# Kernel tuning notes

Hardware: AMD Instinct MI355X
Metric: run time of the kernel (lower is better)

The kernel has to match this reference:

```python
import jax, jax.numpy as jnp
import numpy as np

B, T, C = 2, 2048, 1024
H = 16
DH = C // H  # 64
DFF = 4 * C  # 4096
EPS = 1e-5


def layernorm(x, gamma, beta):
    # torch.var defaults to unbiased (ddof=1) -- replicate exactly
    m = jnp.mean(x, axis=-1, keepdims=True)
    v = jnp.var(x, axis=-1, ddof=1, keepdims=True)
    return (x - m) / jnp.sqrt(v + EPS) * gamma + beta


def setup_inputs() -> dict:
    key = jax.random.key(0)
    ks = jax.random.split(key, 12)
    s = 0.02
    return {
        "x": jax.random.normal(ks[0], (B, T, C), jnp.float32),
        "Wq": jax.random.normal(ks[1], (H, C, DH), jnp.float32) * s,
        "bq": jnp.zeros((H, DH), jnp.float32),
        "Wk": jax.random.normal(ks[2], (H, C, DH), jnp.float32) * s,
        "bk": jnp.zeros((H, DH), jnp.float32),
        "Wv": jax.random.normal(ks[3], (H, C, DH), jnp.float32) * s,
        "bv": jnp.zeros((H, DH), jnp.float32),
        "Wo": jax.random.normal(ks[4], (C, C), jnp.float32) * s,
        "bo": jnp.zeros((C,), jnp.float32),
        "gamma1": jnp.ones((C,), jnp.float32),
        "beta1": jnp.zeros((C,), jnp.float32),
        "gamma2": jnp.ones((C,), jnp.float32),
        "beta2": jnp.zeros((C,), jnp.float32),
        "W1": jax.random.normal(ks[5], (C, DFF), jnp.float32) * s,
        "b1": jnp.zeros((DFF,), jnp.float32),
        "W2": jax.random.normal(ks[6], (DFF, C), jnp.float32) * s,
        "b2": jnp.zeros((C,), jnp.float32),
    }


def reference(x, Wq, bq, Wk, bk, Wv, bv, Wo, bo,
              gamma1, beta1, gamma2, beta2, W1, b1, W2, b2):
    Tn = x.shape[1]
    # Block: x = ln1(x); x = x + attn(x); x = ln2(x); out = x + ffw(x)
    x = layernorm(x, gamma1, beta1)

    # per-head Q/K/V linears, stacked over heads: [B,T,C] x [H,C,Dh] -> [B,H,T,Dh]
    q = jnp.einsum('btc,hcd->bhtd', x, Wq) + bq[None, :, None, :]
    k = jnp.einsum('btc,hcd->bhtd', x, Wk) + bk[None, :, None, :]
    v = jnp.einsum('btc,hcd->bhtd', x, Wv) + bv[None, :, None, :]

    scale = DH ** -0.5
    scores = jnp.einsum('bhtd,bhsd->bhts', q, k) * scale  # [B,H,T,T]
    causal = jnp.tril(jnp.ones((Tn, Tn), dtype=bool))
    scores = jnp.where(causal, scores, -jnp.inf)
    alpha = jax.nn.softmax(scores, axis=-1)
    h = jnp.einsum('bhts,bhsd->bhtd', alpha, v)  # [B,H,T,Dh]
    h = jnp.transpose(h, (0, 2, 1, 3)).reshape(x.shape)  # concat heads -> [B,T,C]
    attn_out = h @ Wo + bo

    x = x + attn_out
    x = layernorm(x, gamma2, beta2)
    ffw = jax.nn.gelu(x @ W1 + b1, approximate=False) @ W2 + b2
    return x + ffw
```

## Files before the change

### kernel.cpp

```cpp
#include <hip/hip_runtime.h>

typedef unsigned short u16;
typedef unsigned int u32;
typedef __attribute__((ext_vector_type(8))) short bf16x8;
typedef __attribute__((ext_vector_type(4))) float f32x4;

#define AS1 __attribute__((address_space(1)))
#define AS3 __attribute__((address_space(3)))

__device__ __forceinline__ u16 f2bf(float f) {
  u32 u = __float_as_uint(f);
  u = (u + 0x7fffu + ((u >> 16) & 1u)) >> 16;
  return (u16)u;
}
__device__ __forceinline__ float bf2f(u16 v) { return __uint_as_float((u32)v << 16); }

__device__ __forceinline__ void gl16(const void* g, void* l) {
  __builtin_amdgcn_global_load_lds((AS1 void*)g, (AS3 void*)l, 16, 0, 0);
}

__device__ __forceinline__ float exp2a(float x) {
  float r;
  asm("v_exp_f32 %0, %1" : "=v"(r) : "v"(x));
  return r;
}
__device__ __forceinline__ u32 pk2(float lo, float hi) {
  u32 r;
  asm("v_cvt_pk_bf16_f32 %0, %1, %2" : "=v"(r) : "v"(lo), "v"(hi));
  return r;
}

#define BAR() __builtin_amdgcn_s_barrier()
#define LGKM0()                                         \
  do {                                                  \
    asm volatile("s_waitcnt lgkmcnt(0)" ::: "memory");  \
    __builtin_amdgcn_sched_barrier(0);                  \
  } while (0)
#define VMC4()                                          \
  do {                                                  \
    asm volatile("s_waitcnt vmcnt(4)" ::: "memory");    \
    __builtin_amdgcn_sched_barrier(0);                  \
  } while (0)
#define VMC0()                                          \
  do {                                                  \
    asm volatile("s_waitcnt vmcnt(0)" ::: "memory");    \
    __builtin_amdgcn_sched_barrier(0);                  \
  } while (0)

__global__ __launch_bounds__(256) void ln_kernel(const float* __restrict__ in,
                                                 const float* __restrict__ gamma,
                                                 const float* __restrict__ beta,
                                                 u16* __restrict__ obf,
                                                 float* __restrict__ of32) {
  const int row = blockIdx.x;
  const int tid = threadIdx.x;
  const float* xr = in + (long)row * 1024;
  float4 v = *(const float4*)(xr + tid * 4);
  float s = v.x + v.y + v.z + v.w;
  float sq = v.x * v.x + v.y * v.y + v.z * v.z + v.w * v.w;
#pragma unroll
  for (int off = 1; off < 64; off <<= 1) {
    s += __shfl_xor(s, off);
    sq += __shfl_xor(sq, off);
  }
  __shared__ float rs[4], rq[4];
  const int w = tid >> 6, lane = tid & 63;
  if (lane == 0) { rs[w] = s; rq[w] = sq; }
  __syncthreads();
  s = rs[0] + rs[1] + rs[2] + rs[3];
  sq = rq[0] + rq[1] + rq[2] + rq[3];
  const float mean = s * (1.0f / 1024.0f);
  const float var = (sq - 1024.0f * mean * mean) * (1.0f / 1023.0f);
  const float rstd = rsqrtf(var + 1e-5f);
  float4 g4 = *(const float4*)(gamma + tid * 4);
  float4 b4 = *(const float4*)(beta + tid * 4);
  float o0 = (v.x - mean) * rstd * g4.x + b4.x;
  float o1 = (v.y - mean) * rstd * g4.y + b4.y;
  float o2 = (v.z - mean) * rstd * g4.z + b4.z;
  float o3 = (v.w - mean) * rstd * g4.w + b4.w;
  *(float4*)(of32 + (long)row * 1024 + tid * 4) = make_float4(o0, o1, o2, o3);
  ushort4 ub;
  ub.x = f2bf(o0); ub.y = f2bf(o1); ub.z = f2bf(o2); ub.w = f2bf(o3);
  *(ushort4*)(obf + (long)row * 1024 + tid * 4) = ub;
}

__global__ __launch_bounds__(256) void ln2_fused_kernel(
    const u16* __restrict__ p0, const u16* __restrict__ p1,
    const float* __restrict__ bo, const float* __restrict__ xn,
    const float* __restrict__ gamma, const float* __restrict__ beta,
    u16* __restrict__ obf, float* __restrict__ of32) {
  const int row = blockIdx.x;
  const int tid = threadIdx.x;
  const long i4 = (long)row * 1024 + tid * 4;
  ushort4 a0 = *(const ushort4*)(p0 + i4);
  ushort4 a1 = *(const ushort4*)(p1 + i4);
  float4 xv = *(const float4*)(xn + i4);
  float4 bv = *(const float4*)(bo + tid * 4);
  float y0 = bf2f(a0.x) + bf2f(a1.x) + bv.x + xv.x;
  float y1 = bf2f(a0.y) + bf2f(a1.y) + bv.y + xv.y;
  float y2 = bf2f(a0.z) + bf2f(a1.z) + bv.z + xv.z;
  float y3 = bf2f(a0.w) + bf2f(a1.w) + bv.w + xv.w;
  float s = y0 + y1 + y2 + y3;
  float sq = y0 * y0 + y1 * y1 + y2 * y2 + y3 * y3;
#pragma unroll
  for (int off = 1; off < 64; off <<= 1) {
    s += __shfl_xor(s, off);
    sq += __shfl_xor(sq, off);
  }
  __shared__ float rs[4], rq[4];
  const int w = tid >> 6, lane = tid & 63;
  if (lane == 0) { rs[w] = s; rq[w] = sq; }
  __syncthreads();
  s = rs[0] + rs[1] + rs[2] + rs[3];
  sq = rq[0] + rq[1] + rq[2] + rq[3];
  const float mean = s * (1.0f / 1024.0f);
  const float var = (sq - 1024.0f * mean * mean) * (1.0f / 1023.0f);
  const float rstd = rsqrtf(var + 1e-5f);
  float4 g4 = *(const float4*)(gamma + tid * 4);
  float4 b4 = *(const float4*)(beta + tid * 4);
  float o0 = (y0 - mean) * rstd * g4.x + b4.x;
  float o1 = (y1 - mean) * rstd * g4.y + b4.y;
  float o2 = (y2 - mean) * rstd * g4.z + b4.z;
  float o3 = (y3 - mean) * rstd * g4.w + b4.w;
  *(float4*)(of32 + i4) = make_float4(o0, o1, o2, o3);
  ushort4 ub;
  ub.x = f2bf(o0); ub.y = f2bf(o1); ub.z = f2bf(o2); ub.w = f2bf(o3);
  *(ushort4*)(obf + i4) = ub;
}

__global__ __launch_bounds__(256) void wtrans_kernel(const float* __restrict__ in,
                                                     u16* __restrict__ out,
                                                     int R, int C, int in_rs,
                                                     long in_batch, long out_batch) {
  __shared__ float tile[32][33];
  const float* ip = in + (long)blockIdx.z * in_batch;
  u16* op = out + (long)blockIdx.z * out_batch;
  const int c0 = blockIdx.x * 32, r0 = blockIdx.y * 32;
  const int tx = threadIdx.x, ty = threadIdx.y;
#pragma unroll
  for (int i = 0; i < 4; ++i)
    tile[ty + i * 8][tx] = ip[(long)(r0 + ty + i * 8) * in_rs + c0 + tx];
  __syncthreads();
#pragma unroll
  for (int i = 0; i < 4; ++i)
    op[(long)(c0 + ty + i * 8) * R + r0 + tx] = f2bf(tile[tx][ty + i * 8]);
}

__device__ __forceinline__ void mfma_phase(f32x4 acc[8][4], const bf16x8 af[4][2],
                                           const bf16x8 bf[2][2], int mq, int nq) {
#pragma unroll
  for (int mf = 0; mf < 4; ++mf)
#pragma unroll
    for (int nf = 0; nf < 2; ++nf)
#pragma unroll
      for (int kh = 0; kh < 2; ++kh)
        acc[mq * 4 + mf][nq * 2 + nf] = __builtin_amdgcn_mfma_f32_16x16x32_bf16(
            af[mf][kh], bf[nf][kh], acc[mq * 4 + mf][nq * 2 + nf], 0, 0, 0);
}

#define STGA(BUFX)                                          \
  do {                                                      \
    gl16(pA0, Asm + (BUFX) * 16384 + tid * 8);              \
    gl16(pA1, Asm + (BUFX) * 16384 + 4096 + tid * 8);       \
    gl16(pA2, Asm + (BUFX) * 16384 + 8192 + tid * 8);       \
    gl16(pA3, Asm + (BUFX) * 16384 + 12288 + tid * 8);      \
  } while (0)
#define STGB(BUFX)                                          \
  do {                                                      \
    gl16(pB0, Bsm + (BUFX) * 16384 + tid * 8);              \
    gl16(pB1, Bsm + (BUFX) * 16384 + 4096 + tid * 8);       \
    gl16(pB2, Bsm + (BUFX) * 16384 + 8192 + tid * 8);       \
    gl16(pB3, Bsm + (BUFX) * 16384 + 12288 + tid * 8);      \
  } while (0)
#define ADVA() do { pA0 += 64; pA1 += 64; pA2 += 64; pA3 += 64; } while (0)
#define ADVB() do { pB0 += 64; pB1 += 64; pB2 += 64; pB3 += 64; } while (0)

#define RD(arr, off) (*(const bf16x8*)((arr) + (off)))

#define KTILE(BUF, T)                                                        \
  do {                                                                       \
    bf16x8 af[4][2], b0[2][2], b1[2][2];                                     \
    _Pragma("unroll") for (int mf = 0; mf < 4; ++mf)                         \
        _Pragma("unroll") for (int kh = 0; kh < 2; ++kh)                     \
            af[mf][kh] = RD(Asm, aO[mf][kh] + (BUF) * 16384);                \
    _Pragma("unroll") for (int nf = 0; nf < 2; ++nf)                         \
        _Pragma("unroll") for (int kh = 0; kh < 2; ++kh)                     \
            b0[nf][kh] = RD(Bsm, bO[nf][kh] + (BUF) * 16384);                \
    if ((T) + 1 < nk) STGA((BUF) ^ 1);                                       \
    BAR(); LGKM0();                                                          \
    __builtin_amdgcn_s_setprio(1);                                           \
    mfma_phase(acc, af, b0, 0, 0);                                           \
    __builtin_amdgcn_s_setprio(0);                                           \
    BAR();                                                                   \
    _Pragma("unroll") for (int nf = 0; nf < 2; ++nf)                         \
        _Pragma("unroll") for (int kh = 0; kh < 2; ++kh)                     \
            b1[nf][kh] = RD(Bsm, bO[nf][kh] + (BUF) * 16384 + 2048);         \
    BAR(); LGKM0();                                                          \
    __builtin_amdgcn_s_setprio(1);                                           \
    mfma_phase(acc, af, b1, 0, 1);                                           \
    __builtin_amdgcn_s_setprio(0);                                           \
    BAR();                                                                   \
    _Pragma("unroll") for (int mf = 0; mf < 4; ++mf)                         \
        _Pragma("unroll") for (int kh = 0; kh < 2; ++kh)                     \
            af[mf][kh] = RD(Asm, aO[mf][kh] + (BUF) * 16384 + 4096);         \
    if ((T) + 2 < nk) STGB(BUF);                                             \
    BAR(); LGKM0();                                                          \
    __builtin_amdgcn_s_setprio(1);                                           \
    mfma_phase(acc, af, b0, 1, 0);                                           \
    __builtin_amdgcn_s_setprio(0);                                           \
    BAR();                                                                   \
    if ((T) + 2 < nk) { VMC4(); } else { VMC0(); }                           \
    BAR();                                                                   \
    __builtin_amdgcn_s_setprio(1);                                           \
    mfma_phase(acc, af, b1, 1, 1);                                           \
    __builtin_amdgcn_s_setprio(0);                                           \
    BAR();                                                                   \
  } while (0)

template <int EPI>
__global__ __launch_bounds__(512, 2) void gemm8_kernel(
    const u16* __restrict__ A, const u16* __restrict__ Bt,
    int lda, int ldb, int M, int N, int nk,
    const float* bias0, const float* bias1, const float* bias2,
    void* out0, void* out1) {
  __shared__ __align__(16) u16 Asm[4 * 8192];
  __shared__ __align__(16) u16 Bsm[4 * 8192];
  const int tid = threadIdx.x;
  const int lane = tid & 63, w = tid >> 6;
  const int wm = w >> 2, wn = w & 3;
  const int q15 = lane & 15, g = lane >> 4;

  const int nbx = gridDim.x, nby = gridDim.y;
  const int nwg = nbx * nby * gridDim.z;
  int lid = blockIdx.x + nbx * (blockIdx.y + nby * blockIdx.z);
  lid = (lid & 7) * (nwg >> 3) + (lid >> 3);
  const int bx = lid % nbx;
  const int rest = lid / nbx;
  const int by = rest % nby;
  const int bz = rest / nby;

  const long m0 = (long)bx * 256;
  const long n0 = (long)by * 256;
  const long koff = (long)bz * (long)nk * 64;
  const u16* Ab = A + m0 * lda + koff;
  const u16* Bb = Bt + n0 * ldb + koff;

  const int jr = tid >> 3;
  const int js = ((tid & 7) ^ (jr & 7)) * 8;
  const u16* pA0 = Ab + (long)jr * lda + js;
  const u16* pA1 = pA0 + (long)64 * lda;
  const u16* pA2 = pA0 + (long)128 * lda;
  const u16* pA3 = pA0 + (long)192 * lda;
  const u16* pB0 = Bb + (long)jr * ldb + js;
  const u16* pB1 = pB0 + (long)64 * ldb;
  const u16* pB2 = pB0 + (long)128 * ldb;
  const u16* pB3 = pB0 + (long)192 * ldb;

  int aO[4][2], bO[2][2];
#pragma unroll
  for (int mf = 0; mf < 4; ++mf)
#pragma unroll
    for (int kh = 0; kh < 2; ++kh) {
      const int rh = mf * 16 + q15;
      aO[mf][kh] = wm * 8192 + rh * 64 + (((kh * 4 + g) ^ (rh & 7)) * 8);
    }
  const int brow = (wn & 1) * 64;
#pragma unroll
  for (int nf = 0; nf < 2; ++nf)
#pragma unroll
    for (int kh = 0; kh < 2; ++kh) {
      const int rh = brow + nf * 16 + q15;
      bO[nf][kh] = (wn >> 1) * 8192 + rh * 64 + (((kh * 4 + g) ^ (rh & 7)) * 8);
    }

  f32x4 acc[8][4];
  f32x4 zero4 = {0.f, 0.f, 0.f, 0.f};
#pragma unroll
  for (int mi = 0; mi < 8; ++mi)
#pragma unroll
    for (int ni = 0; ni < 4; ++ni) acc[mi][ni] = zero4;

  STGA(0);
  STGB(0);
  ADVB();
  if (nk > 1) {
    STGB(1);
    VMC4();
  } else {
    VMC0();
  }
  ADVA();
  ADVB();
  BAR();

  for (int tt = 0; tt < nk; tt += 2) {
    KTILE(0, tt);
    ADVA(); ADVB();
    KTILE(1, tt + 1);
    ADVA(); ADVB();
  }

#pragma unroll
  for (int mi = 0; mi < 8; ++mi) {
#pragma unroll
    for (int ni = 0; ni < 4; ++ni) {
      const long mbase = m0 + wm * 128 + (mi >> 2) * 64 + (mi & 3) * 16 + 4 * g;
      const long n = n0 + wn * 64 + (ni >> 1) * 32 + (ni & 1) * 16 + q15;
      f32x4 a = acc[mi][ni];
      if constexpr (EPI == 0) {
        const int sel = (int)(n >> 10);
        const int nn = (int)(n & 1023);
        const float* bp = sel == 0 ? bias0 : (sel == 1 ? bias1 : bias2);
        const float bb2 = bp[nn];
        if (sel < 2) {
          const float sc = (sel == 0) ? 0.18033688011112043f : 1.0f;
          u16* qkp = (u16*)out0;
#pragma unroll
          for (int r = 0; r < 4; ++r)
            qkp[(mbase + r) * 2048 + n] = f2bf((a[r] + bb2) * sc);
        } else {
          const int bI = (int)(mbase >> 11);
          const int t = (int)(mbase & 2047);
          const int hh = nn >> 6, dh = nn & 63;
          ushort4 pk;
          pk.x = f2bf(a[0] + bb2); pk.y = f2bf(a[1] + bb2);
          pk.z = f2bf(a[2] + bb2); pk.w = f2bf(a[3] + bb2);
          *(ushort4*)((u16*)out1 + ((long)((bI * 16 + hh) * 64 + dh)) * 2048 + t) = pk;
        }
      } else if constexpr (EPI == 2) {
        u16* gp = (u16*)out0;
        const float bb2 = bias0[(int)n];
#pragma unroll
        for (int r = 0; r < 4; ++r) {
          const float xg = a[r] + bb2;
          const float ge = 0.5f * xg * (1.0f + erff(xg * 0.70710678118f));
          gp[(mbase + r) * N + n] = f2bf(ge);
        }
      } else {
        u16* pp = (u16*)out0 + (long)bz * M * N;
#pragma unroll
        for (int r = 0; r < 4; ++r) pp[(mbase + r) * N + n] = f2bf(a[r]);
      }
    }
  }
}

__global__ __launch_bounds__(256) void ffn2_reduce_kernel(const u16* __restrict__ p,
                                                          const float* __restrict__ b2,
                                                          const float* __restrict__ yn,
                                                          float* __restrict__ out) {
  const long i4 = ((long)blockIdx.x * 256 + threadIdx.x) * 4;
  ushort4 p0 = *(const ushort4*)(p + i4);
  ushort4 p1 = *(const ushort4*)(p + 4194304 + i4);
  ushort4 p2 = *(const ushort4*)(p + 8388608 + i4);
  ushort4 p3 = *(const ushort4*)(p + 12582912 + i4);
  float4 rr = *(const float4*)(yn + i4);
  const int nn = (int)(i4 & 1023);
  float4 bb = *(const float4*)(b2 + nn);
  float4 o;
  o.x = bf2f(p0.x) + bf2f(p1.x) + bf2f(p2.x) + bf2f(p3.x) + bb.x + rr.x;
  o.y = bf2f(p0.y) + bf2f(p1.y) + bf2f(p2.y) + bf2f(p3.y) + bb.y + rr.y;
  o.z = bf2f(p0.z) + bf2f(p1.z) + bf2f(p2.z) + bf2f(p3.z) + bb.z + rr.z;
  o.w = bf2f(p0.w) + bf2f(p1.w) + bf2f(p2.w) + bf2f(p3.w) + bb.w + rr.w;
  *(float4*)(out + i4) = o;
}

__global__ __launch_bounds__(256, 2) void gemm_wo_kernel(const u16* __restrict__ A,
                                                         const u16* __restrict__ Bt,
                                                         u16* __restrict__ part) {
  __shared__ __align__(16) u16 Asm[128 * 64];
  __shared__ __align__(16) u16 Bsm[128 * 64];
  const int tid = threadIdx.x;
  const int lane = tid & 63, w = tid >> 6;
  const int wm = w >> 1, wn = w & 1;
  const int q = lane & 15, g = lane >> 4;
  const long m0 = (long)blockIdx.x * 128;
  const long n0 = (long)blockIdx.y * 128;
  const int bz = blockIdx.z;
  const long koff = (long)bz * 512;

  f32x4 zero4 = {0.f, 0.f, 0.f, 0.f};
  f32x4 acc[4][4];
#pragma unroll
  for (int mi = 0; mi < 4; ++mi)
#pragma unroll
    for (int ni = 0; ni < 4; ++ni) acc[mi][ni] = zero4;

  for (int ks = 0; ks < 8; ++ks) {
    __syncthreads();
    const u16* ga = A + m0 * 1024 + koff + ks * 64;
    const u16* gb = Bt + n0 * 1024 + koff + ks * 64;
    const int base = w * 256;
#pragma unroll
    for (int i = 0; i < 4; ++i) {
      const int idx = base + i * 64 + lane;
      const int row = idx >> 3;
      const int lg = (idx & 7) ^ (row & 7);
      gl16(ga + (long)row * 1024 + lg * 8, Asm + (long)(base + i * 64) * 8);
    }
#pragma unroll
    for (int i = 0; i < 4; ++i) {
      const int idx = base + i * 64 + lane;
      const int row = idx >> 3;
      const int lg = (idx & 7) ^ (row & 7);
      gl16(gb + (long)row * 1024 + lg * 8, Bsm + (long)(base + i * 64) * 8);
    }
    __syncthreads();
#pragma unroll
    for (int half = 0; half < 2; ++half) {
      bf16x8 af[4], bfv[4];
#pragma unroll
      for (int mi = 0; mi < 4; ++mi) {
        const int row = wm * 64 + mi * 16 + q;
        const int ph = (half * 4 + g) ^ (row & 7);
        af[mi] = *(const bf16x8*)(Asm + row * 64 + ph * 8);
      }
#pragma unroll
      for (int ni = 0; ni < 4; ++ni) {
        const int row = wn * 64 + ni * 16 + q;
        const int ph = (half * 4 + g) ^ (row & 7);
        bfv[ni] = *(const bf16x8*)(Bsm + row * 64 + ph * 8);
      }
#pragma unroll
      for (int mi = 0; mi < 4; ++mi)
#pragma unroll
        for (int ni = 0; ni < 4; ++ni)
          acc[mi][ni] = __builtin_amdgcn_mfma_f32_16x16x32_bf16(af[mi], bfv[ni],
                                                                acc[mi][ni], 0, 0, 0);
    }
  }
  u16* pp = part + (long)bz * 4096 * 1024;
#pragma unroll
  for (int mi = 0; mi < 4; ++mi) {
#pragma unroll
    for (int ni = 0; ni < 4; ++ni) {
      const long mbase = m0 + wm * 64 + mi * 16 + 4 * g;
      const long n = n0 + wn * 64 + ni * 16 + q;
      f32x4 a = acc[mi][ni];
#pragma unroll
      for (int r = 0; r < 4; ++r) pp[(mbase + r) * 1024 + n] = f2bf(a[r]);
    }
  }
}

__device__ __forceinline__ void attn_stage(const u16* kbase, const u16* vtb, int kb,
                                           u16* Kd, u16* Vd, int tid) {
#pragma unroll
  for (int it = 0; it < 2; ++it) {
    const int j = it * 256 + tid;
    const int row = j >> 3;
    const int lg = (j & 7) ^ (row & 7);
    gl16(kbase + (long)(kb * 64 + row) * 2048 + lg * 8, Kd + j * 8);
    gl16(vtb + (long)row * 2048 + kb * 64 + lg * 8, Vd + j * 8);
  }
}

__device__ __forceinline__ void softmax_slab(const f32x4 st[4], bool diag, int qrow,
                                             int kb, int g, int q15,
                                             float& m2, float& l, u16* prow,
                                             float al[4]) {
  float sv[4][4];
  float rmax = -1e30f;
#pragma unroll
  for (int sub = 0; sub < 4; ++sub)
#pragma unroll
    for (int r = 0; r < 4; ++r) {
      float s_ = st[sub][r];
      if (diag) {
        const int key = kb * 64 + sub * 16 + 4 * g + r;
        s_ = (key > qrow) ? -1e30f : s_;
      }
      sv[sub][r] = s_;
      rmax = fmaxf(rmax, s_);
    }
  rmax = fmaxf(rmax, __shfl_xor(rmax, 16));
  rmax = fmaxf(rmax, __shfl_xor(rmax, 32));
  const float mnew = fmaxf(m2, rmax);
  const float alpha = exp2a(m2 - mnew);
  float psum = 0.f;
#pragma unroll
  for (int sub = 0; sub < 4; ++sub) {
    const float p0 = exp2a(sv[sub][0] - mnew);
    const float p1 = exp2a(sv[sub][1] - mnew);
    const float p2 = exp2a(sv[sub][2] - mnew);
    const float p3 = exp2a(sv[sub][3] - mnew);
    uint2 u;
    u.x = pk2(p0, p1);
    u.y = pk2(p2, p3);
    *(uint2*)(prow + sub * 16 + 4 * g) = u;
    psum += (p0 + p1) + (p2 + p3);
  }
  psum += __shfl_xor(psum, 16);
  psum += __shfl_xor(psum, 32);
  l = l * alpha + psum;
  m2 = mnew;
#pragma unroll
  for (int r = 0; r < 4; ++r) al[r] = __shfl(alpha, 4 * g + r);
}

__global__ __launch_bounds__(256, 2) void attn_kernel(const u16* __restrict__ qk,
                                                      const u16* __restrict__ vT,
                                                      u16* __restrict__ o) {
  __shared__ __align__(16) u16 Ksm[2][64 * 64];
  __shared__ __align__(16) u16 Vsm[2][64 * 64];
  __shared__ __align__(16) u16 Psm[8][16][72];
  const int lid = blockIdx.x;
  const int xcd = lid & 7, s6 = lid >> 3;
  const int b2 = (s6 >> 4) & 3, xr = s6 & 15;
  const int qs = (b2 & 2) ? (15 - xr) : xr;
  const int bh = xcd + 8 * b2;
  const int b = bh >> 4, h = bh & 15;
  const int tid = threadIdx.x, lane = tid & 63, w = tid >> 6;
  const int q15 = lane & 15, g = lane >> 4;
  const u16* qbase = qk + (long)b * 2048 * 2048 + h * 64;
  const u16* kbase = qbase + 1024;
  const u16* vtb = vT + (long)bh * 64 * 2048;
  f32x4 zero4 = {0.f, 0.f, 0.f, 0.f};

  const int r0 = qs * 128 + w * 16 + q15;
  bf16x8 qa[2][2];
  qa[0][0] = *(const bf16x8*)(qbase + (long)r0 * 2048 + g * 8);
  qa[0][1] = *(const bf16x8*)(qbase + (long)r0 * 2048 + 32 + g * 8);
  qa[1][0] = *(const bf16x8*)(qbase + (long)(r0 + 64) * 2048 + g * 8);
  qa[1][1] = *(const bf16x8*)(qbase + (long)(r0 + 64) * 2048 + 32 + g * 8);

  f32x4 oa0[4], oa1[4];
#pragma unroll
  for (int dv = 0; dv < 4; ++dv) { oa0[dv] = zero4; oa1[dv] = zero4; }
  float m20 = -1e30f, l0 = 0.f, m21 = -1e30f, l1 = 0.f;
  const int kbmax = 2 * qs + 1;

  attn_stage(kbase, vtb, 0, Ksm[0], Vsm[0], tid);
  VMC0();
  __syncthreads();

  for (int kb = 0; kb <= kbmax; ++kb) {
    const int buf = kb & 1;
    if (kb < kbmax) attn_stage(kbase, vtb, kb + 1, Ksm[buf ^ 1], Vsm[buf ^ 1], tid);
    const u16* Kb = Ksm[buf];
    const u16* Vb = Vsm[buf];
    const bool s0on = (kb <= 2 * qs);
    f32x4 st0[4], st1[4];
#pragma unroll
    for (int sub = 0; sub < 4; ++sub) {
      const int row = sub * 16 + q15;
      const bf16x8 ka0 = *(const bf16x8*)(Kb + row * 64 + ((g ^ (row & 7)) * 8));
      const bf16x8 ka1 = *(const bf16x8*)(Kb + row * 64 + (((4 + g) ^ (row & 7)) * 8));
      f32x4 z = zero4;
      z = __builtin_amdgcn_mfma_f32_16x16x32_bf16(ka0, qa[1][0], z, 0, 0, 0);
      z = __builtin_amdgcn_mfma_f32_16x16x32_bf16(ka1, qa[1][1], z, 0, 0, 0);
      st1[sub] = z;
      if (s0on) {
        f32x4 z0 = zero4;
        z0 = __builtin_amdgcn_mfma_f32_16x16x32_bf16(ka0, qa[0][0], z0, 0, 0, 0);
        z0 = __builtin_amdgcn_mfma_f32_16x16x32_bf16(ka1, qa[0][1], z0, 0, 0, 0);
        st0[sub] = z0;
      }
    }
    float al0[4], al1[4];
    if (s0on)
      softmax_slab(st0, kb == 2 * qs, r0, kb, g, q15, m20, l0, &Psm[w * 2][q15][0], al0);
    softmax_slab(st1, kb == 2 * qs + 1, r0 + 64, kb, g, q15, m21, l1,
                 &Psm[w * 2 + 1][q15][0], al1);
    if (s0on)
#pragma unroll
      for (int dv = 0; dv < 4; ++dv) {
        oa0[dv][0] *= al0[0]; oa0[dv][1] *= al0[1];
        oa0[dv][2] *= al0[2]; oa0[dv][3] *= al0[3];
      }
#pragma unroll
    for (int dv = 0; dv < 4; ++dv) {
      oa1[dv][0] *= al1[0]; oa1[dv][1] *= al1[1];
      oa1[dv][2] *= al1[2]; oa1[dv][3] *= al1[3];
    }
    LGKM0();
#pragma unroll
    for (int half = 0; half < 2; ++half) {
      const bf16x8 pa0 = *(const bf16x8*)(&Psm[w * 2][q15][half * 32 + 8 * g]);
      const bf16x8 pa1 = *(const bf16x8*)(&Psm[w * 2 + 1][q15][half * 32 + 8 * g]);
#pragma unroll
      for (int dv = 0; dv < 4; ++dv) {
        const int row = dv * 16 + q15;
        const bf16x8 vb = *(const bf16x8*)(Vb + row * 64 + (((half * 4 + g) ^ (row & 7)) * 8));
        if (s0on) oa0[dv] = __builtin_amdgcn_mfma_f32_16x16x32_bf16(pa0, vb, oa0[dv], 0, 0, 0);
        oa1[dv] = __builtin_amdgcn_mfma_f32_16x16x32_bf16(pa1, vb, oa1[dv], 0, 0, 0);
      }
    }
    VMC0();
    __syncthreads();
  }
  const float li0 = 1.0f / l0, li1 = 1.0f / l1;
  float v0[4], v1[4];
#pragma unroll
  for (int r = 0; r < 4; ++r) {
    v0[r] = __shfl(li0, 4 * g + r);
    v1[r] = __shfl(li1, 4 * g + r);
  }
  const int tok0 = b * 2048 + qs * 128 + w * 16;
#pragma unroll
  for (int dv = 0; dv < 4; ++dv)
#pragma unroll
    for (int r = 0; r < 4; ++r) {
      o[(long)(tok0 + 4 * g + r) * 1024 + h * 64 + dv * 16 + q15] =
          f2bf(oa0[dv][r] * v0[r]);
      o[(long)(tok0 + 64 + 4 * g + r) * 1024 + h * 64 + dv * 16 + q15] =
          f2bf(oa1[dv][r] * v1[r]);
    }
}

extern "C" void kernel_launch(void* const* d_in, const int* in_sizes, int n_in,
                              void* d_out, int out_size, void* d_ws, size_t ws_size,
                              hipStream_t stream) {
  (void)in_sizes; (void)n_in; (void)out_size; (void)ws_size;
  const float* x  = (const float*)d_in[0];
  const float* Wq = (const float*)d_in[1];
  const float* bq = (const float*)d_in[2];
  const float* Wk = (const float*)d_in[3];
  const float* bk = (const float*)d_in[4];
  const float* Wv = (const float*)d_in[5];
  const float* bv = (const float*)d_in[6];
  const float* Wo = (const float*)d_in[7];
  const float* bo = (const float*)d_in[8];
  const float* g1 = (const float*)d_in[9];
  const float* be1 = (const float*)d_in[10];
  const float* g2 = (const float*)d_in[11];
  const float* be2 = (const float*)d_in[12];
  const float* W1 = (const float*)d_in[13];
  const float* b1 = (const float*)d_in[14];
  const float* W2 = (const float*)d_in[15];
  const float* b2 = (const float*)d_in[16];

  char* ws = (char*)d_ws;
  u16*   xn_bf = (u16*)  (ws + 0);
  float* xn_f  = (float*)(ws + 8388608);
  u16*   WqkvT = (u16*)  (ws + 25165824);
  u16*   WoT   = (u16*)  (ws + 31457280);
  u16*   W1T   = (u16*)  (ws + 33554432);
  u16*   W2T   = (u16*)  (ws + 41943040);
  u16*   qkb   = (u16*)  (ws + 50331648);
  u16*   vTb   = (u16*)  (ws + 67108864);
  u16*   ah    = (u16*)  (ws + 75497472);
  u16*   pwo0  = (u16*)  (ws + 50331648);
  u16*   pwo1  = (u16*)  (ws + 58720256);
  u16*   gbuf  = (u16*)  (ws + 50331648);
  u16*   part  = (u16*)  (ws + 0);
  u16*   yn_bf = (u16*)  (ws + 83886080);
  float* yn_f  = (float*)(ws + 92274688);

  dim3 tb(32, 8), b256(256), b512(512);
  wtrans_kernel<<<dim3(2, 32, 16), tb, 0, stream>>>(Wq, WqkvT,            1024, 64, 64, 65536l, 65536l);
  wtrans_kernel<<<dim3(2, 32, 16), tb, 0, stream>>>(Wk, WqkvT + 1048576,  1024, 64, 64, 65536l, 65536l);
  wtrans_kernel<<<dim3(2, 32, 16), tb, 0, stream>>>(Wv, WqkvT + 2097152,  1024, 64, 64, 65536l, 65536l);
  wtrans_kernel<<<dim3(32, 32, 1),  tb, 0, stream>>>(Wo, WoT, 1024, 1024, 1024, 0l, 0l);
  wtrans_kernel<<<dim3(128, 32, 1), tb, 0, stream>>>(W1, W1T, 1024, 4096, 4096, 0l, 0l);
  wtrans_kernel<<<dim3(32, 128, 1), tb, 0, stream>>>(W2, W2T, 4096, 1024, 1024, 0l, 0l);
  ln_kernel<<<dim3(4096), b256, 0, stream>>>(x, g1, be1, xn_bf, xn_f);
  gemm8_kernel<0><<<dim3(16, 12, 1), b512, 0, stream>>>(xn_bf, WqkvT, 1024, 1024,
                                                        4096, 3072, 16, bq, bk, bv, qkb, vTb);
  attn_kernel<<<dim3(512), b256, 0, stream>>>(qkb, vTb, ah);
  gemm_wo_kernel<<<dim3(32, 8, 2), b256, 0, stream>>>(ah, WoT, pwo0);
  ln2_fused_kernel<<<dim3(4096), b256, 0, stream>>>(pwo0, pwo1, bo, xn_f, g2, be2,
                                                    yn_bf, yn_f);
  gemm8_kernel<2><<<dim3(16, 16, 1), b512, 0, stream>>>(yn_bf, W1T, 1024, 1024,
                                                        4096, 4096, 16, b1, nullptr, nullptr, gbuf, nullptr);
  gemm8_kernel<4><<<dim3(16, 4, 4), b512, 0, stream>>>(gbuf, W2T, 4096, 4096,
                                                       4096, 1024, 16, nullptr, nullptr, nullptr, part, nullptr);
  ffn2_reduce_kernel<<<dim3(4096), b256, 0, stream>>>(part, b2, yn_f, (float*)d_out);
}
```

Baseline: 245.0 us.

## Simplify GEMM k-loop to plain double buffering with one barrier per tile

Replaces the staggered A/B prefetch schedule, with its interleaved barriers, priority bumps and partial vmcnt waits, with a simpler double-buffered loop. Each k-tile now loads all B fragments up front, issues the next tile's A and B prefetch together, runs all four MFMA phases back to back, then waits on vmcnt(0) and takes a single barrier. The aim is to remove barrier and setprio overhead per tile. In exchange, the full wait at the end of each tile limits how much memory latency can hide behind compute, and more B registers stay live at once.

```diff
diff --git a/kernel.cpp b/kernel.cpp
--- a/kernel.cpp
+++ b/kernel.cpp
@@ -34,11 +34,6 @@
 #define LGKM0()                                         \
   do {                                                  \
     asm volatile("s_waitcnt lgkmcnt(0)" ::: "memory");  \
-    __builtin_amdgcn_sched_barrier(0);                  \
-  } while (0)
-#define VMC4()                                          \
-  do {                                                  \
-    asm volatile("s_waitcnt vmcnt(4)" ::: "memory");    \
     __builtin_amdgcn_sched_barrier(0);                  \
   } while (0)
 #define VMC0()                                          \
@@ -177,43 +172,28 @@
 
 #define RD(arr, off) (*(const bf16x8*)((arr) + (off)))
 
-#define KTILE(BUF, T)                                                        \
+#define KTILE2(BUF, T)                                                       \
   do {                                                                       \
-    bf16x8 af[4][2], b0[2][2], b1[2][2];                                     \
+    bf16x8 af[4][2], bv0[2][2], bv1[2][2];                                   \
     _Pragma("unroll") for (int mf = 0; mf < 4; ++mf)                         \
         _Pragma("unroll") for (int kh = 0; kh < 2; ++kh)                     \
             af[mf][kh] = RD(Asm, aO[mf][kh] + (BUF) * 16384);                \
     _Pragma("unroll") for (int nf = 0; nf < 2; ++nf)                         \
-        _Pragma("unroll") for (int kh = 0; kh < 2; ++kh)                     \
-            b0[nf][kh] = RD(Bsm, bO[nf][kh] + (BUF) * 16384);                \
-    if ((T) + 1 < nk) STGA((BUF) ^ 1);                                       \
-    BAR(); LGKM0();                                                          \
-    __builtin_amdgcn_s_setprio(1);                                           \
-    mfma_phase(acc, af, b0, 0, 0);                                           \
-    __builtin_amdgcn_s_setprio(0);                                           \
-    BAR();                                                                   \
-    _Pragma("unroll") for (int nf = 0; nf < 2; ++nf)                         \
-        _Pragma("unroll") for (int kh = 0; kh < 2; ++kh)                     \
-            b1[nf][kh] = RD(Bsm, bO[nf][kh] + (BUF) * 16384 + 2048);         \
-    BAR(); LGKM0();                                                          \
-    __builtin_amdgcn_s_setprio(1);                                           \
-    mfma_phase(acc, af, b1, 0, 1);                                           \
-    __builtin_amdgcn_s_setprio(0);                                           \
-    BAR();                                                                   \
+        _Pragma("unroll") for (int kh = 0; kh < 2; ++kh) {                   \
+      bv0[nf][kh] = RD(Bsm, bO[nf][kh] + (BUF) * 16384);                     \
+      bv1[nf][kh] = RD(Bsm, bO[nf][kh] + (BUF) * 16384 + 2048);              \
+    }                                                                        \
+    if ((T) + 1 < nk) { STGA((BUF) ^ 1); STGB((BUF) ^ 1); }                  \
+    LGKM0();                                                                 \
+    mfma_phase(acc, af, bv0, 0, 0);                                          \
+    mfma_phase(acc, af, bv1, 0, 1);                                          \
     _Pragma("unroll") for (int mf = 0; mf < 4; ++mf)                         \
         _Pragma("unroll") for (int kh = 0; kh < 2; ++kh)                     \
             af[mf][kh] = RD(Asm, aO[mf][kh] + (BUF) * 16384 + 4096);         \
-    if ((T) + 2 < nk) STGB(BUF);                                             \
-    BAR(); LGKM0();                                                          \
-    __builtin_amdgcn_s_setprio(1);                                           \
-    mfma_phase(acc, af, b0, 1, 0);                                           \
-    __builtin_amdgcn_s_setprio(0);                                           \
-    BAR();                                                                   \
-    if ((T) + 2 < nk) { VMC4(); } else { VMC0(); }                           \
-    BAR();                                                                   \
-    __builtin_amdgcn_s_setprio(1);                                           \
-    mfma_phase(acc, af, b1, 1, 1);                                           \
-    __builtin_amdgcn_s_setprio(0);                                           \
+    LGKM0();                                                                 \
+    mfma_phase(acc, af, bv0, 1, 0);                                          \
+    mfma_phase(acc, af, bv1, 1, 1);                                          \
+    if ((T) + 1 < nk) VMC0();                                                \
     BAR();                                                                   \
   } while (0)
 
@@ -282,21 +262,15 @@
 
   STGA(0);
   STGB(0);
-  ADVB();
-  if (nk > 1) {
-    STGB(1);
-    VMC4();
-  } else {
-    VMC0();
-  }
   ADVA();
   ADVB();
+  VMC0();
   BAR();
 
   for (int tt = 0; tt < nk; tt += 2) {
-    KTILE(0, tt);
+    KTILE2(0, tt);
     ADVA(); ADVB();
-    KTILE(1, tt + 1);
+    KTILE2(1, tt + 1);
     ADVA(); ADVB();
   }
 
```

Result: faster. 239.4 us (-2.3%).
